# Optimization experiments

Hardware: AMD Instinct MI355X
Metric: run time of the kernel (lower is better)

Reference implementation:

```python
import jax, jax.numpy as jnp
import numpy as np

B, S, H, I, R = 4, 256, 4096, 14336, 4

def setup_inputs() -> dict:
    key = jax.random.key(0)
    ks = jax.random.split(key, 10)
    sd = 0.02
    return {
        "x": jax.random.normal(ks[0], (B, S, H), dtype=jnp.float32),
        "gate_w": jax.random.normal(ks[1], (I, H), dtype=jnp.float32) * sd,
        "gate_su": jax.random.normal(ks[2], (I, R), dtype=jnp.float32) * 0.5,
        "gate_sv": jax.random.normal(ks[3], (R, H), dtype=jnp.float32) * 0.5,
        "up_w": jax.random.normal(ks[4], (I, H), dtype=jnp.float32) * sd,
        "up_su": jax.random.normal(ks[5], (I, R), dtype=jnp.float32) * 0.5,
        "up_sv": jax.random.normal(ks[6], (R, H), dtype=jnp.float32) * 0.5,
        "down_w": jax.random.normal(ks[7], (H, I), dtype=jnp.float32) * sd,
        "down_su": jax.random.normal(ks[8], (H, R), dtype=jnp.float32) * 0.5,
        "down_sv": jax.random.normal(ks[9], (R, I), dtype=jnp.float32) * 0.5,
    }

def _anemll_linear(x, w, su, sv):
    # AnemllConv2d: 1x1 conv whose effective weight is the stored (quantized)
    # base weight modulated by a rank-R scale matrix: W_eff = w * (su @ sv).
    # x: [b, s, in], w: [out, in], su: [out, R], sv: [R, in] -> [b, s, out]
    w_eff = w * (su @ sv)
    return jnp.einsum('bsh,oh->bso', x, w_eff)

def reference(x, gate_w, gate_su, gate_sv, up_w, up_su, up_sv, down_w, down_su, down_sv):
    # Qwen MLP: down( silu(gate(x)) * up(x) )
    a = _anemll_linear(x, gate_w, gate_su, gate_sv)   # [B,S,I]
    b = _anemll_linear(x, up_w, up_su, up_sv)         # [B,S,I]
    d = jax.nn.silu(a) * b                            # fused SwiGLU
    return _anemll_linear(d, down_w, down_su, down_sv)  # [B,S,H]
```

## Files before the change

kernel.cpp:

```cpp
#include <hip/hip_runtime.h>
#include <hip/hip_bf16.h>

typedef __bf16 bf16;
typedef __attribute__((ext_vector_type(4))) __bf16 bf16x4;
typedef __attribute__((ext_vector_type(8))) __bf16 bf16x8;
typedef __attribute__((ext_vector_type(4))) float f32x4;
typedef __attribute__((ext_vector_type(16))) float f32x16;

__device__ __forceinline__ void async_load16(const bf16* g, const bf16* l) {
    __builtin_amdgcn_global_load_lds(
        (const __attribute__((address_space(1))) unsigned int*)g,
        (__attribute__((address_space(3))) unsigned int*)l,
        16, 0, 0);
}

__global__ void cvt_bf16_kernel(const float* __restrict__ in, bf16* __restrict__ out) {
    const int i = blockIdx.x * blockDim.x + threadIdx.x;
    const f32x4* p = (const f32x4*)in + (size_t)i * 2;
    f32x4 a = p[0], b = p[1];
    bf16x8 o;
    o[0] = (bf16)a[0]; o[1] = (bf16)a[1]; o[2] = (bf16)a[2]; o[3] = (bf16)a[3];
    o[4] = (bf16)b[0]; o[5] = (bf16)b[1]; o[6] = (bf16)b[2]; o[7] = (bf16)b[3];
    *((bf16x8*)out + (size_t)i) = o;
}

__global__ __launch_bounds__(256)
void dequant_kernel(const float* __restrict__ W, const float* __restrict__ SU,
                    const float* __restrict__ SV, bf16* __restrict__ out, const int K) {
    const int n  = blockIdx.y;
    const int c4 = blockIdx.x * blockDim.x + threadIdx.x;
    const size_t base = (size_t)n * K + (size_t)c4 * 4;
    f32x4 w  = *(const f32x4*)(W + base);
    f32x4 s0 = *(const f32x4*)(SV + (size_t)0 * K + c4 * 4);
    f32x4 s1 = *(const f32x4*)(SV + (size_t)1 * K + c4 * 4);
    f32x4 s2 = *(const f32x4*)(SV + (size_t)2 * K + c4 * 4);
    f32x4 s3 = *(const f32x4*)(SV + (size_t)3 * K + c4 * 4);
    f32x4 su = *(const f32x4*)(SU + (size_t)n * 4);
    bf16x4 o;
#pragma unroll
    for (int j = 0; j < 4; ++j) {
        float sc = su[0] * s0[j] + su[1] * s1[j] + su[2] * s2[j] + su[3] * s3[j];
        o[j] = (bf16)(w[j] * sc);
    }
    *(bf16x4*)(out + base) = o;
}

template<int BM, int KDIM, int NMAT>
__global__ __launch_bounds__(256, 2)
void gemm_bf16(const bf16* __restrict__ A,
               const bf16* __restrict__ B0, const bf16* __restrict__ B1,
               void* __restrict__ OUTp, const int NT)
{
    constexpr int BK  = 32;
    constexpr int BN  = 64;
    constexpr int NI  = BN / 32;
    constexpr int RPW = BM / 4;
    constexpr int MI  = RPW / 32;
    constexpr int NLD = RPW / 16;
    constexpr int KIT = KDIM / BK;

    __shared__ bf16 sA[2][BM * BK];
    __shared__ bf16 sB[2][NMAT][BN * BK];

    const int tid  = threadIdx.x;
    const int lane = tid & 63;
    const int wv   = tid >> 6;
    const int m0   = blockIdx.x * BM;
    const int n0   = blockIdx.y * BN;

    const int aseg = (lane & 3) ^ ((lane >> 4) & 3);
    const bf16* gA  = A  + (size_t)(m0 + wv * RPW + (lane >> 2)) * KDIM + aseg * 8;
    const bf16* gB0 = B0 + (size_t)(n0 + wv * 16 + (lane >> 2)) * KDIM + aseg * 8;
    const bf16* gB1 = nullptr;
    if constexpr (NMAT == 2)
        gB1 = B1 + (size_t)(n0 + wv * 16 + (lane >> 2)) * KDIM + aseg * 8;

    f32x16 acc[NMAT][NI][MI];
#pragma unroll
    for (int mt = 0; mt < NMAT; ++mt)
#pragma unroll
        for (int ni = 0; ni < NI; ++ni)
#pragma unroll
            for (int mi = 0; mi < MI; ++mi)
#pragma unroll
                for (int r = 0; r < 16; ++r)
                    acc[mt][ni][mi][r] = 0.0f;

    auto stage = [&](int k0, int buf) {
#pragma unroll
        for (int i = 0; i < NLD; ++i)
            async_load16(gA + (size_t)i * 16 * KDIM + k0,
                         &sA[buf][(wv * RPW + i * 16) * BK]);
        async_load16(gB0 + k0, &sB[buf][0][(wv * 16) * BK]);
        if constexpr (NMAT == 2)
            async_load16(gB1 + k0, &sB[buf][1][(wv * 16) * BK]);
    };

    const int il = lane & 31;
    const int xr = (il >> 2) & 3;
    const int hi = lane >> 5;

    stage(0, 0);
    __syncthreads();

    for (int kt = 0; kt < KIT; ++kt) {
        const int cb = kt & 1, nb = cb ^ 1;
        if (kt + 1 < KIT) stage((kt + 1) * BK, nb);

#pragma unroll
        for (int t = 0; t < BK / 16; ++t) {
            const int ksl = ((t * 2 + hi) ^ xr) * 8;
            bf16x8 af[MI];
#pragma unroll
            for (int mi = 0; mi < MI; ++mi)
                af[mi] = *(const bf16x8*)(&sA[cb][(wv * RPW + mi * 32 + il) * BK + ksl]);
#pragma unroll
            for (int mt = 0; mt < NMAT; ++mt)
#pragma unroll
                for (int ni = 0; ni < NI; ++ni) {
                    bf16x8 bv = *(const bf16x8*)(&sB[cb][mt][(ni * 32 + il) * BK + ksl]);
#pragma unroll
                    for (int mi = 0; mi < MI; ++mi)
                        acc[mt][ni][mi] = __builtin_amdgcn_mfma_f32_32x32x16_bf16(
                            af[mi], bv, acc[mt][ni][mi], 0, 0, 0);
                }
        }
        __syncthreads();
    }

    const int rq = hi * 4;
#pragma unroll
    for (int ni = 0; ni < NI; ++ni)
#pragma unroll
        for (int mi = 0; mi < MI; ++mi)
#pragma unroll
            for (int r = 0; r < 16; ++r) {
                const int row = m0 + wv * RPW + mi * 32 + rq + (r & 3) + ((r >> 2) << 3);
                const size_t idx = (size_t)row * NT + (n0 + ni * 32 + il);
                if constexpr (NMAT == 2) {
                    const float g = acc[0][ni][mi][r];
                    const float u = acc[1][ni][mi][r];
                    ((bf16*)OUTp)[idx] = (bf16)(g / (1.0f + __expf(-g)) * u);
                } else {
                    ((float*)OUTp)[idx] = acc[0][ni][mi][r];
                }
            }
}

template<int BM, int KDIM, int NMAT>
__global__ __launch_bounds__(256, 2)
void mlp_gemm(const bf16* __restrict__ A,
              const float* __restrict__ W0, const float* __restrict__ SU0, const float* __restrict__ SV0,
              const float* __restrict__ W1, const float* __restrict__ SU1, const float* __restrict__ SV1,
              void* __restrict__ OUTp, const int NT)
{
    constexpr int BK  = 32;
    constexpr int BN  = 32;
    constexpr int RPW = BM / 4;
    constexpr int MI  = RPW / 32;
    constexpr int NLD = RPW / 16;
    constexpr int SBS = BK + 8;
    constexpr int KIT = KDIM / BK;

    __shared__ bf16 sA[2][BM * BK];
    __shared__ bf16 sB[2][NMAT][BN * SBS];

    const int tid  = threadIdx.x;
    const int lane = tid & 63;
    const int wv   = tid >> 6;
    const int m0   = blockIdx.x * BM;
    const int n0   = blockIdx.y * BN;

    const int aseg = (lane & 3) ^ ((lane >> 4) & 3);
    const bf16* gA = A + (size_t)(m0 + wv * RPW + (lane >> 2)) * KDIM + aseg * 8;

    const int brow = tid >> 3;
    const int bseg = tid & 7;
    const float* gW0  = W0 + (size_t)(n0 + brow) * KDIM + bseg * 4;
    const float* gSV0 = SV0 + bseg * 4;
    const f32x4  su0  = *(const f32x4*)(SU0 + (size_t)(n0 + brow) * 4);
    const float* gW1  = nullptr; const float* gSV1 = nullptr; f32x4 su1{};
    if constexpr (NMAT == 2) {
        gW1  = W1 + (size_t)(n0 + brow) * KDIM + bseg * 4;
        gSV1 = SV1 + bseg * 4;
        su1  = *(const f32x4*)(SU1 + (size_t)(n0 + brow) * 4);
    }
    const int sboff = brow * SBS + bseg * 4;

    f32x16 acc[NMAT][MI];
#pragma unroll
    for (int mt = 0; mt < NMAT; ++mt)
#pragma unroll
        for (int mi = 0; mi < MI; ++mi)
#pragma unroll
            for (int r = 0; r < 16; ++r)
                acc[mt][mi][r] = 0.0f;

    f32x4 w0r{}, s00{}, s01{}, s02{}, s03{};
    f32x4 w1r{}, s10{}, s11{}, s12{}, s13{};

    auto loadW = [&](int k0) {
        w0r = *(const f32x4*)(gW0 + k0);
        s00 = *(const f32x4*)(gSV0 + k0);
        s01 = *(const f32x4*)(gSV0 + KDIM + k0);
        s02 = *(const f32x4*)(gSV0 + 2 * KDIM + k0);
        s03 = *(const f32x4*)(gSV0 + 3 * KDIM + k0);
        if constexpr (NMAT == 2) {
            w1r = *(const f32x4*)(gW1 + k0);
            s10 = *(const f32x4*)(gSV1 + k0);
            s11 = *(const f32x4*)(gSV1 + KDIM + k0);
            s12 = *(const f32x4*)(gSV1 + 2 * KDIM + k0);
            s13 = *(const f32x4*)(gSV1 + 3 * KDIM + k0);
        }
    };

    auto stageA = [&](int k0, int buf) {
#pragma unroll
        for (int i = 0; i < NLD; ++i)
            async_load16(gA + (size_t)i * 16 * KDIM + k0,
                         &sA[buf][(wv * RPW + i * 16) * BK]);
    };

    auto dequant = [&](int buf) {
        bf16x4 ov;
#pragma unroll
        for (int j = 0; j < 4; ++j) {
            float sc = su0[0] * s00[j] + su0[1] * s01[j] + su0[2] * s02[j] + su0[3] * s03[j];
            ov[j] = (bf16)(w0r[j] * sc);
        }
        *(bf16x4*)&sB[buf][0][sboff] = ov;
        if constexpr (NMAT == 2) {
            bf16x4 ov1;
#pragma unroll
            for (int j = 0; j < 4; ++j) {
                float sc = su1[0] * s10[j] + su1[1] * s11[j] + su1[2] * s12[j] + su1[3] * s13[j];
                ov1[j] = (bf16)(w1r[j] * sc);
            }
            *(bf16x4*)&sB[buf][1][sboff] = ov1;
        }
    };

    const int xr = ((lane & 31) >> 2) & 3;
    const int hi = lane >> 5;

    loadW(0);
    stageA(0, 0);
    dequant(0);
    __syncthreads();

    for (int kt = 0; kt < KIT; ++kt) {
        const int cb = kt & 1, nb = cb ^ 1;
        const bool more = (kt + 1 < KIT);

        if (more) {
            loadW((kt + 1) * BK);
            stageA((kt + 1) * BK, nb);
        }

#pragma unroll
        for (int t = 0; t < BK / 16; ++t) {
            bf16x8 af[MI];
#pragma unroll
            for (int mi = 0; mi < MI; ++mi)
                af[mi] = *(const bf16x8*)(&sA[cb][(wv * RPW + mi * 32 + (lane & 31)) * BK
                                                  + (((t * 2 + hi) ^ xr) * 8)]);
#pragma unroll
            for (int mt = 0; mt < NMAT; ++mt) {
                bf16x8 bv = *(const bf16x8*)(&sB[cb][mt][(lane & 31) * SBS
                                                         + t * 16 + hi * 8]);
#pragma unroll
                for (int mi = 0; mi < MI; ++mi)
                    acc[mt][mi] = __builtin_amdgcn_mfma_f32_32x32x16_bf16(
                        af[mi], bv, acc[mt][mi], 0, 0, 0);
            }
        }

        if (more) dequant(nb);
        __syncthreads();
    }

    const int cbl = lane & 31;
    const int rq  = (lane >> 5) * 4;
#pragma unroll
    for (int mi = 0; mi < MI; ++mi)
#pragma unroll
        for (int r = 0; r < 16; ++r) {
            const int row = m0 + wv * RPW + mi * 32 + rq + (r & 3) + ((r >> 2) << 3);
            const size_t idx = (size_t)row * NT + (n0 + cbl);
            if constexpr (NMAT == 2) {
                const float g = acc[0][mi][r];
                const float u = acc[1][mi][r];
                const float d = g / (1.0f + __expf(-g)) * u;
                ((bf16*)OUTp)[idx] = (bf16)d;
            } else {
                ((float*)OUTp)[idx] = acc[0][mi][r];
            }
        }
}

extern "C" void kernel_launch(void* const* d_in, const int* in_sizes, int n_in,
                              void* d_out, int out_size, void* d_ws, size_t ws_size,
                              hipStream_t stream) {
    (void)in_sizes; (void)n_in; (void)out_size;

    const float* x   = (const float*)d_in[0];
    const float* gw  = (const float*)d_in[1];
    const float* gsu = (const float*)d_in[2];
    const float* gsv = (const float*)d_in[3];
    const float* uw  = (const float*)d_in[4];
    const float* usu = (const float*)d_in[5];
    const float* usv = (const float*)d_in[6];
    const float* dw  = (const float*)d_in[7];
    const float* dsu = (const float*)d_in[8];
    const float* dsv = (const float*)d_in[9];

    const size_t XBF = (size_t)1024 * 4096 * 2;
    const size_t DSW = (size_t)1024 * 14336 * 2;
    const size_t WSZ = (size_t)14336 * 4096 * 2;
    const size_t REQ = XBF + DSW + 3 * WSZ;

    bf16* x_bf = (bf16*)d_ws;
    bf16* d_sw = (bf16*)((char*)d_ws + XBF);
    float* out = (float*)d_out;

    cvt_bf16_kernel<<<2048, 256, 0, stream>>>(x, x_bf);

    if (ws_size >= REQ) {
        bf16* Wg = (bf16*)((char*)d_ws + XBF + DSW);
        bf16* Wu = (bf16*)((char*)Wg + WSZ);
        bf16* Wd = (bf16*)((char*)Wu + WSZ);

        dequant_kernel<<<dim3(4, 14336), 256, 0, stream>>>(gw, gsu, gsv, Wg, 4096);
        dequant_kernel<<<dim3(4, 14336), 256, 0, stream>>>(uw, usu, usv, Wu, 4096);
        dequant_kernel<<<dim3(14, 4096), 256, 0, stream>>>(dw, dsu, dsv, Wd, 14336);

        gemm_bf16<256, 4096, 2><<<dim3(4, 224), 256, 0, stream>>>(
            x_bf, Wg, Wu, d_sw, 14336);

        gemm_bf16<128, 14336, 1><<<dim3(8, 64), 256, 0, stream>>>(
            d_sw, Wd, nullptr, out, 4096);
    } else {
        mlp_gemm<512, 4096, 2><<<dim3(2, 448), 256, 0, stream>>>(
            x_bf, gw, gsu, gsv, uw, usu, usv, d_sw, 14336);
        mlp_gemm<512, 14336, 1><<<dim3(2, 128), 256, 0, stream>>>(
            d_sw, dw, dsu, dsv, nullptr, nullptr, nullptr, out, 4096);
    }
}
```

Measured before the change: 1.399 ms.

## Deepen GEMM pipeline to multi-buffered LDS with vmcnt waits and XCD-aware block remap

Replaces the double-buffered GEMM loop with an NBUF-stage ring of async global-to-LDS loads. Each stage waits on an explicit s_waitcnt vmcnt count instead of a full __syncthreads, so several tiles stay in flight. Block IDs are remapped across the 8 XCDs so that neighbouring tiles share L2. The down-projection also moves to BK=64 with a matching swizzle. The extra buffers raise LDS use, which may limit occupancy, and the hand-written waitcnt and barrier logic is fragile.

```diff
diff --git a/kernel.cpp b/kernel.cpp
--- a/kernel.cpp
+++ b/kernel.cpp
@@ -12,6 +12,17 @@
         (const __attribute__((address_space(1))) unsigned int*)g,
         (__attribute__((address_space(3))) unsigned int*)l,
         16, 0, 0);
+}
+
+template<int N>
+__device__ __forceinline__ void wait_vmcnt() {
+    asm volatile("s_waitcnt vmcnt(%0)" :: "n"(N) : "memory");
+}
+__device__ __forceinline__ void fence_lgkm0() {
+    asm volatile("s_waitcnt lgkmcnt(0)" ::: "memory");
+}
+__device__ __forceinline__ void barrier_mem() {
+    asm volatile("s_barrier" ::: "memory");
 }
 
 __global__ void cvt_bf16_kernel(const float* __restrict__ in, bf16* __restrict__ out) {
@@ -45,35 +56,48 @@
     *(bf16x4*)(out + base) = o;
 }
 
-template<int BM, int KDIM, int NMAT>
+template<int BM, int BK, int KDIM, int NMAT, int NBUF, int GXLOG>
 __global__ __launch_bounds__(256, 2)
 void gemm_bf16(const bf16* __restrict__ A,
                const bf16* __restrict__ B0, const bf16* __restrict__ B1,
                void* __restrict__ OUTp, const int NT)
 {
-    constexpr int BK  = 32;
-    constexpr int BN  = 64;
-    constexpr int NI  = BN / 32;
-    constexpr int RPW = BM / 4;
-    constexpr int MI  = RPW / 32;
-    constexpr int NLD = RPW / 16;
-    constexpr int KIT = KDIM / BK;
-
-    __shared__ bf16 sA[2][BM * BK];
-    __shared__ bf16 sB[2][NMAT][BN * BK];
+    constexpr int BN    = 64;
+    constexpr int NI    = 2;
+    constexpr int RPW   = BM / 4;
+    constexpr int MI    = RPW / 32;
+    constexpr int SEGS  = BK / 8;
+    constexpr int RPI   = 64 / SEGS;
+    constexpr int NLD   = RPW / RPI;
+    constexpr int BLD   = 16 / RPI;
+    constexpr int LTOT  = NLD + NMAT * BLD;
+    constexpr int KIT   = KDIM / BK;
+    static_assert(NBUF >= 2 && NBUF <= 4, "wait chain covers NBUF 2..4");
+    static_assert(NBUF * LTOT <= 63, "vmcnt range");
+
+    __shared__ __align__(16) bf16 sA[NBUF][BM * BK];
+    __shared__ __align__(16) bf16 sB[NBUF][NMAT][BN * BK];
 
     const int tid  = threadIdx.x;
     const int lane = tid & 63;
     const int wv   = tid >> 6;
-    const int m0   = blockIdx.x * BM;
-    const int n0   = blockIdx.y * BN;
-
-    const int aseg = (lane & 3) ^ ((lane >> 4) & 3);
-    const bf16* gA  = A  + (size_t)(m0 + wv * RPW + (lane >> 2)) * KDIM + aseg * 8;
-    const bf16* gB0 = B0 + (size_t)(n0 + wv * 16 + (lane >> 2)) * KDIM + aseg * 8;
+
+    const int nwg = gridDim.x;
+    const int lid = (blockIdx.x & 7) * (nwg >> 3) + (blockIdx.x >> 3);
+    const int m0  = (lid & ((1 << GXLOG) - 1)) * BM;
+    const int n0  = (lid >> GXLOG) * BN;
+
+    const int srow = lane / SEGS;
+    const int sseg = lane % SEGS;
+    int aseg;
+    if constexpr (BK == 32) aseg = sseg ^ ((lane >> 4) & 3);
+    else                    aseg = sseg ^ (srow & 7);
+
+    const bf16* gA  = A  + (size_t)(m0 + wv * RPW + srow) * KDIM + aseg * 8;
+    const bf16* gB0 = B0 + (size_t)(n0 + wv * 16  + srow) * KDIM + aseg * 8;
     const bf16* gB1 = nullptr;
     if constexpr (NMAT == 2)
-        gB1 = B1 + (size_t)(n0 + wv * 16 + (lane >> 2)) * KDIM + aseg * 8;
+        gB1 = B1 + (size_t)(n0 + wv * 16 + srow) * KDIM + aseg * 8;
 
     f32x16 acc[NMAT][NI][MI];
 #pragma unroll
@@ -86,30 +110,46 @@
                 for (int r = 0; r < 16; ++r)
                     acc[mt][ni][mi][r] = 0.0f;
 
-    auto stage = [&](int k0, int buf) {
+    auto stage = [&](int kt, int buf) {
+        const int k0 = kt * BK;
 #pragma unroll
         for (int i = 0; i < NLD; ++i)
-            async_load16(gA + (size_t)i * 16 * KDIM + k0,
-                         &sA[buf][(wv * RPW + i * 16) * BK]);
-        async_load16(gB0 + k0, &sB[buf][0][(wv * 16) * BK]);
-        if constexpr (NMAT == 2)
-            async_load16(gB1 + k0, &sB[buf][1][(wv * 16) * BK]);
+            async_load16(gA + (size_t)i * RPI * KDIM + k0,
+                         &sA[buf][(wv * RPW + i * RPI) * BK]);
+#pragma unroll
+        for (int j = 0; j < BLD; ++j) {
+            async_load16(gB0 + (size_t)j * RPI * KDIM + k0,
+                         &sB[buf][0][(wv * 16 + j * RPI) * BK]);
+            if constexpr (NMAT == 2)
+                async_load16(gB1 + (size_t)j * RPI * KDIM + k0,
+                             &sB[buf][1][(wv * 16 + j * RPI) * BK]);
+        }
+    };
+
+    auto wait_tile = [&](int rem) {
+        if (rem >= NBUF - 1) { wait_vmcnt<(NBUF - 1) * LTOT>(); return; }
+        if constexpr (NBUF >= 4) { if (rem == 2) { wait_vmcnt<2 * LTOT>(); return; } }
+        if constexpr (NBUF >= 3) { if (rem == 1) { wait_vmcnt<1 * LTOT>(); return; } }
+        wait_vmcnt<0>();
     };
 
     const int il = lane & 31;
-    const int xr = (il >> 2) & 3;
     const int hi = lane >> 5;
-
-    stage(0, 0);
-    __syncthreads();
-
+    int xrk;
+    if constexpr (BK == 32) xrk = (il >> 2) & 3;
+    else                    xrk = il & 7;
+
+#pragma unroll
+    for (int p = 0; p < NBUF; ++p) stage(p, p);
+
+    int cb = 0;
     for (int kt = 0; kt < KIT; ++kt) {
-        const int cb = kt & 1, nb = cb ^ 1;
-        if (kt + 1 < KIT) stage((kt + 1) * BK, nb);
+        wait_tile(KIT - 1 - kt);
+        barrier_mem();
 
 #pragma unroll
         for (int t = 0; t < BK / 16; ++t) {
-            const int ksl = ((t * 2 + hi) ^ xr) * 8;
+            const int ksl = ((t * 2 + hi) ^ xrk) * 8;
             bf16x8 af[MI];
 #pragma unroll
             for (int mi = 0; mi < MI; ++mi)
@@ -125,7 +165,11 @@
                             af[mi], bv, acc[mt][ni][mi], 0, 0, 0);
                 }
         }
-        __syncthreads();
+
+        fence_lgkm0();
+        barrier_mem();
+        if (kt + NBUF < KIT) stage(kt + NBUF, cb);
+        cb = (cb + 1 == NBUF) ? 0 : cb + 1;
     }
 
     const int rq = hi * 4;
@@ -334,10 +378,10 @@
         dequant_kernel<<<dim3(4, 14336), 256, 0, stream>>>(uw, usu, usv, Wu, 4096);
         dequant_kernel<<<dim3(14, 4096), 256, 0, stream>>>(dw, dsu, dsv, Wd, 14336);
 
-        gemm_bf16<256, 4096, 2><<<dim3(4, 224), 256, 0, stream>>>(
+        gemm_bf16<256, 32, 4096, 2, 3, 2><<<896, 256, 0, stream>>>(
             x_bf, Wg, Wu, d_sw, 14336);
 
-        gemm_bf16<128, 14336, 1><<<dim3(8, 64), 256, 0, stream>>>(
+        gemm_bf16<128, 64, 14336, 1, 3, 3><<<512, 256, 0, stream>>>(
             d_sw, Wd, nullptr, out, 4096);
     } else {
         mlp_gemm<512, 4096, 2><<<dim3(2, 448), 256, 0, stream>>>(
```

Result: faster. 1.206 ms (-13.8%).
